# Performance work log

Measured on AMD Instinct MI355X. Metric: run time of the kernel, lower is better.

The kernel has to match this reference:

```python
import jax, jax.numpy as jnp
import numpy as np

D_MODEL = 512
N_HEADS = 8
EDGE_FEAT_DIM = 4
NUM_GRAPHS = 64
NODES_PER_GRAPH = 128
N_NODES = NUM_GRAPHS * NODES_PER_GRAPH          # 8192
EDGES_PER_GRAPH = 4096                           # avg degree 32
N_EDGES = NUM_GRAPHS * EDGES_PER_GRAPH           # 262144


def setup_inputs() -> dict:
    key = jax.random.key(0)
    ks = jax.random.split(key, 12)
    s = 0.02
    x = jax.random.normal(ks[0], (N_NODES, D_MODEL), jnp.float32)
    # edges constrained within their graph (block-diagonal structure)
    g_of_e = jnp.arange(N_EDGES, dtype=jnp.int32) // EDGES_PER_GRAPH
    src = g_of_e * NODES_PER_GRAPH + jax.random.randint(ks[1], (N_EDGES,), 0, NODES_PER_GRAPH, jnp.int32)
    dst = g_of_e * NODES_PER_GRAPH + jax.random.randint(ks[2], (N_EDGES,), 0, NODES_PER_GRAPH, jnp.int32)
    edge_index = jnp.stack([src, dst]).astype(jnp.int32)
    edge_attr = jax.random.normal(ks[3], (N_EDGES, EDGE_FEAT_DIM), jnp.float32)
    batch = jnp.repeat(jnp.arange(NUM_GRAPHS, dtype=jnp.int32), NODES_PER_GRAPH)
    # projection weights (in,out) convention: y = x @ W + b
    Wq = jax.random.normal(ks[4], (D_MODEL, D_MODEL), jnp.float32) * s
    Wk = jax.random.normal(ks[5], (D_MODEL, D_MODEL), jnp.float32) * s
    Wv = jax.random.normal(ks[6], (D_MODEL, D_MODEL), jnp.float32) * s
    Wo = jax.random.normal(ks[7], (D_MODEL, D_MODEL), jnp.float32) * s
    bq = jnp.zeros((D_MODEL,), jnp.float32)
    bk = jnp.zeros((D_MODEL,), jnp.float32)
    bv = jnp.zeros((D_MODEL,), jnp.float32)
    bo = jnp.zeros((D_MODEL,), jnp.float32)
    # edge bias MLP: edge_feat_dim -> d_model -> n_heads
    W1 = jax.random.normal(ks[8], (EDGE_FEAT_DIM, D_MODEL), jnp.float32) * s
    b1 = jnp.zeros((D_MODEL,), jnp.float32)
    W2 = jax.random.normal(ks[9], (D_MODEL, N_HEADS), jnp.float32) * s
    b2 = jnp.zeros((N_HEADS,), jnp.float32)
    return {"x": x, "edge_index": edge_index, "edge_attr": edge_attr, "batch": batch,
            "n_g": NODES_PER_GRAPH,
            "Wq": Wq, "bq": bq, "Wk": Wk, "bk": bk, "Wv": Wv, "bv": bv,
            "Wo": Wo, "bo": bo, "W1": W1, "b1": b1, "W2": W2, "b2": b2}


def reference(x, edge_index, edge_attr, batch, n_g, Wq, bq, Wk, bk, Wv, bv, Wo, bo, W1, b1, W2, b2):
    # batch is contiguous equal-size blocks of n_g nodes per graph, so the
    # per-graph Python loop of the original collapses to a batched (G, n_g)
    # block-diagonal attention. Dropout is identity (eval / p used only in train).
    N, d_model = x.shape
    H = W2.shape[1]
    d_k = d_model // H
    G = N // n_g
    scale = 1.0 / float(np.sqrt(d_k))

    Q = (x @ Wq + bq).reshape(G, n_g, H, d_k)
    K = (x @ Wk + bk).reshape(G, n_g, H, d_k)
    V = (x @ Wv + bv).reshape(G, n_g, H, d_k)

    # (G, i, j, h) dense per-graph scores
    scores = jnp.einsum('gihd,gjhd->gijh', Q, K) * scale

    # edge bias: MLP(edge_attr) -> (E, H), scattered at (graph, local_src, local_dst)
    bias = jax.nn.relu(edge_attr @ W1 + b1) @ W2 + b2
    ge = edge_index[0] // n_g
    ls = edge_index[0] % n_g
    ld = edge_index[1] % n_g
    scores = scores.at[ge, ls, ld].add(bias)

    attn = jax.nn.softmax(scores, axis=2)  # softmax over j (keys), matches dim=1 of (i,j,h)
    out = jnp.einsum('gijh,gjhd->gihd', attn, V).reshape(N, d_model)
    return out @ Wo + bo
```

## Files before the change

### kernel.cpp

```cpp
#include <hip/hip_runtime.h>
#include <hip/hip_bf16.h>

#define E_TOTAL 262144
#define NG      128
#define GRAPHS  64
#define NHEADS  8
#define DKH     64
#define DMODEL  512
#define NNODES  8192

typedef __bf16 bf16x8 __attribute__((ext_vector_type(8)));
typedef __bf16 bf16x4 __attribute__((ext_vector_type(4)));
typedef float  f32x4  __attribute__((ext_vector_type(4)));
typedef short  s16x4  __attribute__((ext_vector_type(4)));

typedef __attribute__((address_space(3))) char lds_char;
typedef const __attribute__((address_space(1))) char glb_char;

__device__ inline __hip_bfloat16 f2hbf(float f) { return __float2bfloat16(f); }
__device__ inline unsigned short f2u16(float f) {
    return __builtin_bit_cast(unsigned short, __float2bfloat16(f));
}
__device__ inline __bf16 f2bf(float f) {
    return __builtin_bit_cast(__bf16, f2u16(f));
}
__device__ inline bf16x8 cvt8(float4 lo, float4 hi) {
    bf16x8 o;
    o[0] = f2bf(lo.x); o[1] = f2bf(lo.y); o[2] = f2bf(lo.z); o[3] = f2bf(lo.w);
    o[4] = f2bf(hi.x); o[5] = f2bf(hi.y); o[6] = f2bf(hi.z); o[7] = f2bf(hi.w);
    return o;
}

__global__ __launch_bounds__(256) void prep_kernel(
    const float* __restrict__ Wq, const float* __restrict__ Wk,
    const float* __restrict__ Wv, const float* __restrict__ Wo,
    const float* __restrict__ W1, const float* __restrict__ b1,
    const float* __restrict__ W2, const float* __restrict__ b2,
    const float* __restrict__ x, __hip_bfloat16* __restrict__ xbf,
    __hip_bfloat16* __restrict__ wqkvt, __hip_bfloat16* __restrict__ wot,
    __hip_bfloat16* __restrict__ w1fragt, float* __restrict__ b1f,
    __hip_bfloat16* __restrict__ w2at, float* __restrict__ b2f)
{
    int blk = blockIdx.x, tid = threadIdx.x;
    if (blk < 256) {
        __shared__ __align__(16) __hip_bfloat16 tile[64][65];
        const float* src;
        __hip_bfloat16* dstT;
        int n0, k0, nb;
        if (blk < 192) {
            int nt = blk % 24, ktile = blk / 24;
            n0 = nt * 64; k0 = ktile * 64;
            if (n0 < 512)       { src = Wq; nb = n0; }
            else if (n0 < 1024) { src = Wk; nb = n0 - 512; }
            else                { src = Wv; nb = n0 - 1024; }
            dstT = wqkvt;
        } else {
            int t = blk - 192;
            n0 = (t % 8) * 64; k0 = (t / 8) * 64; nb = n0;
            src = Wo; dstT = wot;
        }
        #pragma unroll
        for (int i = 0; i < 16; ++i) {
            int idx = tid + i * 256;
            int kr = idx >> 6, nc = idx & 63;
            tile[kr][nc] = f2hbf(src[(size_t)(k0 + kr) * 512 + nb + nc]);
        }
        __syncthreads();
        #pragma unroll
        for (int i = 0; i < 16; ++i) {
            int idx = tid + i * 256;
            int nr = idx >> 6, kc = idx & 63;
            dstT[(size_t)(n0 + nr) * 512 + k0 + kc] = tile[kc][nr];
        }
    } else if (blk == 256) {
        __hip_bfloat16 z = f2hbf(0.f);
        for (int n = tid; n < 512; n += 256) {
            #pragma unroll
            for (int j = 0; j < 4; ++j) w1fragt[n * 4 + j] = f2hbf(W1[(size_t)j * 512 + n]);
        }
        for (int i = tid; i < 512; i += 256) b1f[i] = b1[i];
        for (int i = tid; i < 32 * 64 * 4; i += 256) {
            int t = i >> 8, lane = (i >> 2) & 63, j = i & 3;
            int q = lane >> 4, l = lane & 15;
            w2at[i] = (l < 8) ? f2hbf(W2[(size_t)(16 * t + 4 * q + j) * 8 + l]) : z;
        }
        if (tid < 8) b2f[tid] = b2[tid];
    } else {
        int base = (blk - 257) * 2048 + tid * 8;
        float4 lo = *(const float4*)(x + base);
        float4 hi = *(const float4*)(x + base + 4);
        *(bf16x8*)(xbf + base) = cvt8(lo, hi);
    }
}

template <bool QKPATH>
__device__ __forceinline__ void gemm0_body(
    const __hip_bfloat16* __restrict__ A, const __hip_bfloat16* __restrict__ BT,
    int row0, int col0,
    const float* __restrict__ bq, const float* __restrict__ bk,
    const float* __restrict__ bv,
    __hip_bfloat16* __restrict__ qbuf, __hip_bfloat16* __restrict__ kbuf,
    __hip_bfloat16* __restrict__ vt,
    __hip_bfloat16* __restrict__ As, __hip_bfloat16* __restrict__ Bs)
{
    const int K = 512;
    int tid = threadIdx.x;
    int lane = tid & 63, quad = lane >> 4, l16 = lane & 15;
    int wave = tid >> 6;
    int wi = wave >> 1, wj = wave & 1;

    f32x4 acc[2][4];
    #pragma unroll
    for (int a = 0; a < 2; a++)
        #pragma unroll
        for (int b = 0; b < 4; b++)
            #pragma unroll
            for (int r = 0; r < 4; r++) acc[a][b][r] = 0.f;

    const __hip_bfloat16* Ag = A + (size_t)(row0 + (tid >> 2)) * K + (tid & 3) * 8;
    const __hip_bfloat16* Bg = BT + (size_t)(col0 + (tid >> 2)) * K + (tid & 3) * 8;
    char* AsB = (char*)As;
    char* BsB = (char*)Bs;

#define G0STAGE(kt, buf) do { \
    __builtin_amdgcn_global_load_lds((glb_char*)(Ag + (kt) * 32), (lds_char*)(AsB + (buf) * 8192 + tid * 16), 16, 0, 0); \
    __builtin_amdgcn_global_load_lds((glb_char*)(Bg + (kt) * 32), (lds_char*)(BsB + (buf) * 8192 + tid * 16), 16, 0, 0); \
} while (0)

    G0STAGE(0, 0);
    G0STAGE(1, 1);

    #pragma unroll
    for (int kt = 0; kt < 16; ++kt) {
        if (kt < 15) asm volatile("s_waitcnt vmcnt(2)" ::: "memory");
        else         asm volatile("s_waitcnt vmcnt(0)" ::: "memory");
        __builtin_amdgcn_s_barrier();
        if (kt < 14) G0STAGE(kt + 2, (kt + 2) % 3);
        const __hip_bfloat16* Asc = As + (kt % 3) * 4096;
        const __hip_bfloat16* Bsc = Bs + (kt % 3) * 4096;
        bf16x8 af[2], bfr[4];
        #pragma unroll
        for (int t = 0; t < 2; t++)
            af[t] = *(const bf16x8*)&Asc[(wi * 32 + t * 16 + l16) * 32 + quad * 8];
        #pragma unroll
        for (int t = 0; t < 4; t++)
            bfr[t] = *(const bf16x8*)&Bsc[(wj * 64 + t * 16 + l16) * 32 + quad * 8];
        #pragma unroll
        for (int ti = 0; ti < 2; ti++)
            #pragma unroll
            for (int tj = 0; tj < 4; tj++) {
                if constexpr (QKPATH)
                    acc[ti][tj] = __builtin_amdgcn_mfma_f32_16x16x32_bf16(bfr[tj], af[ti], acc[ti][tj], 0, 0, 0);
                else
                    acc[ti][tj] = __builtin_amdgcn_mfma_f32_16x16x32_bf16(af[ti], bfr[tj], acc[ti][tj], 0, 0, 0);
            }
    }
#undef G0STAGE

    if constexpr (QKPATH) {
        int g = row0 >> 7;
        int ibase = wi * 32 + l16;
        int cb0 = col0 + wj * 64 + quad * 4;
        bool isQ = (col0 < 512);
        const float* bias = isQ ? bq : bk;
        int boff = isQ ? 0 : 512;
        __hip_bfloat16* dstbuf = isQ ? qbuf : kbuf;
        #pragma unroll
        for (int tj = 0; tj < 4; tj++) {
            int cb = cb0 + tj * 16;
            float4 bb = *(const float4*)(bias + cb - boff);
            int c = cb - boff;
            int hh = c >> 6, d = c & 63;
            __hip_bfloat16* dst = dstbuf + ((size_t)(g * 8 + hh) * 128) * 64 + d;
            #pragma unroll
            for (int ti = 0; ti < 2; ti++) {
                int i = ibase + ti * 16;
                bf16x4 v;
                v[0] = f2bf(acc[ti][tj][0] + bb.x);
                v[1] = f2bf(acc[ti][tj][1] + bb.y);
                v[2] = f2bf(acc[ti][tj][2] + bb.z);
                v[3] = f2bf(acc[ti][tj][3] + bb.w);
                *(bf16x4*)(dst + (size_t)i * 64) = v;
            }
        }
    } else {
        int g = row0 >> 7;
        int i0 = wi * 32 + quad * 4;
        #pragma unroll
        for (int tj = 0; tj < 4; tj++) {
            int c = col0 - 1024 + wj * 64 + tj * 16 + l16;
            int hh = c >> 6, d = c & 63;
            float bvv = bv[c];
            __hip_bfloat16* vdst = vt + ((size_t)(g * 8 + hh) * 64 + d) * 128 + i0;
            #pragma unroll
            for (int ti = 0; ti < 2; ti++) {
                bf16x4 v;
                v[0] = f2bf(acc[ti][tj][0] + bvv);
                v[1] = f2bf(acc[ti][tj][1] + bvv);
                v[2] = f2bf(acc[ti][tj][2] + bvv);
                v[3] = f2bf(acc[ti][tj][3] + bvv);
                *(bf16x4*)(vdst + ti * 16) = v;
            }
        }
    }
}

__device__ __forceinline__ void edge_body(
    int eblk,
    const float* __restrict__ ea,
    const __hip_bfloat16* __restrict__ w1fragt, const float* __restrict__ b1f,
    const __hip_bfloat16* __restrict__ w2at, const float* __restrict__ b2f,
    float* __restrict__ biasE)
{
    int tid = threadIdx.x, wave = tid >> 6, lane = tid & 63;
    int quad = lane >> 4, l16 = lane & 15;
    int eb = eblk * 512 + wave * 64;

    s16x4 eaf[4] = {};
    if (quad == 0) {
        #pragma unroll
        for (int gg = 0; gg < 4; ++gg) {
            float4 e4 = *(const float4*)(ea + (size_t)(eb + gg * 16 + l16) * 4);
            eaf[gg][0] = (short)f2u16(e4.x); eaf[gg][1] = (short)f2u16(e4.y);
            eaf[gg][2] = (short)f2u16(e4.z); eaf[gg][3] = (short)f2u16(e4.w);
        }
    }

    f32x4 c2[4];
    #pragma unroll
    for (int gg = 0; gg < 4; ++gg)
        #pragma unroll
        for (int r = 0; r < 4; ++r) c2[gg][r] = 0.f;

    #pragma unroll 4
    for (int t = 0; t < 32; ++t) {
        s16x4 a1 = *(const s16x4*)(w1fragt + ((size_t)t * 16 + l16) * 4);
        float4 b14 = *(const float4*)(b1f + t * 16 + quad * 4);
        s16x4 a2 = *(const s16x4*)(w2at + ((size_t)t * 64 + lane) * 4);
        #pragma unroll
        for (int gg = 0; gg < 4; ++gg) {
            f32x4 c1;
            c1[0] = b14.x; c1[1] = b14.y; c1[2] = b14.z; c1[3] = b14.w;
            c1 = __builtin_amdgcn_mfma_f32_16x16x16bf16_1k(a1, eaf[gg], c1, 0, 0, 0);
            s16x4 hfrag;
            hfrag[0] = (short)f2u16(fmaxf(c1[0], 0.f));
            hfrag[1] = (short)f2u16(fmaxf(c1[1], 0.f));
            hfrag[2] = (short)f2u16(fmaxf(c1[2], 0.f));
            hfrag[3] = (short)f2u16(fmaxf(c1[3], 0.f));
            c2[gg] = __builtin_amdgcn_mfma_f32_16x16x16bf16_1k(a2, hfrag, c2[gg], 0, 0, 0);
        }
    }
    if (quad < 2) {
        #pragma unroll
        for (int gg = 0; gg < 4; ++gg) {
            #pragma unroll
            for (int r = 0; r < 4; ++r) {
                int hh = quad * 4 + r;
                biasE[(size_t)hh * E_TOTAL + eb + gg * 16 + l16] = c2[gg][r] + b2f[hh];
            }
        }
    }
}

__global__ __launch_bounds__(512) void mega_kernel(
    const __hip_bfloat16* __restrict__ A, const __hip_bfloat16* __restrict__ BT,
    const float* __restrict__ bq, const float* __restrict__ bk,
    const float* __restrict__ bv,
    __hip_bfloat16* __restrict__ qbuf, __hip_bfloat16* __restrict__ kbuf,
    __hip_bfloat16* __restrict__ vt,
    const float* __restrict__ ea,
    const __hip_bfloat16* __restrict__ w1fragt, const float* __restrict__ b1f,
    const __hip_bfloat16* __restrict__ w2at, const float* __restrict__ b2f,
    float* __restrict__ biasE)
{
    __shared__ __align__(16) __hip_bfloat16 As[3 * 128 * 32];
    __shared__ __align__(16) __hip_bfloat16 Bs[3 * 128 * 32];
    int blk = blockIdx.x;
    int u = blk / 5, v = blk % 5;
    if (v < 3) {
        int tile = u * 3 + v;
        int row0 = (tile & 63) * 128, col0 = (tile >> 6) * 128;
        if (col0 < 1024)
            gemm0_body<true>(A, BT, row0, col0, bq, bk, bv, qbuf, kbuf, vt, As, Bs);
        else
            gemm0_body<false>(A, BT, row0, col0, bq, bk, bv, qbuf, kbuf, vt, As, Bs);
    } else {
        edge_body(u * 2 + (v - 3), ea, w1fragt, b1f, w2at, b2f, biasE);
    }
}

__global__ __launch_bounds__(256) void gemm1_kernel(
    const __hip_bfloat16* __restrict__ A, const __hip_bfloat16* __restrict__ BT,
    const float* __restrict__ bo, float* __restrict__ out)
{
    const int K = 512;
    __shared__ __align__(16) __hip_bfloat16 As[3 * 128 * 32];
    __shared__ __align__(16) __hip_bfloat16 Bs[3 * 64 * 32];
    int tid = threadIdx.x;
    int lane = tid & 63, quad = lane >> 4, l16 = lane & 15;
    int wave = tid >> 6, wi = wave >> 1, wj = wave & 1;
    int row0 = blockIdx.x * 128, col0 = blockIdx.y * 64;

    f32x4 acc[4][2];
    #pragma unroll
    for (int a = 0; a < 4; a++)
        #pragma unroll
        for (int b = 0; b < 2; b++)
            #pragma unroll
            for (int r = 0; r < 4; r++) acc[a][b][r] = 0.f;

    const __hip_bfloat16* Ag0 = A + (size_t)(row0 + (tid >> 2)) * K + (tid & 3) * 8;
    const __hip_bfloat16* Ag1 = Ag0 + (size_t)64 * K;
    const __hip_bfloat16* Bg  = BT + (size_t)(col0 + (tid >> 2)) * K + (tid & 3) * 8;
    char* AsB = (char*)As;
    char* BsB = (char*)Bs;

#define G1STAGE(kt, buf) do { \
    __builtin_amdgcn_global_load_lds((glb_char*)(Ag0 + (kt) * 32), (lds_char*)(AsB + (buf) * 8192 + tid * 16), 16, 0, 0); \
    __builtin_amdgcn_global_load_lds((glb_char*)(Ag1 + (kt) * 32), (lds_char*)(AsB + (buf) * 8192 + 4096 + tid * 16), 16, 0, 0); \
    __builtin_amdgcn_global_load_lds((glb_char*)(Bg + (kt) * 32),  (lds_char*)(BsB + (buf) * 4096 + tid * 16), 16, 0, 0); \
} while (0)

    G1STAGE(0, 0);
    G1STAGE(1, 1);

    #pragma unroll
    for (int kt = 0; kt < 16; ++kt) {
        if (kt < 15) asm volatile("s_waitcnt vmcnt(3)" ::: "memory");
        else         asm volatile("s_waitcnt vmcnt(0)" ::: "memory");
        __builtin_amdgcn_s_barrier();
        if (kt < 14) G1STAGE(kt + 2, (kt + 2) % 3);
        const __hip_bfloat16* Asc = As + (kt % 3) * 4096;
        const __hip_bfloat16* Bsc = Bs + (kt % 3) * 2048;
        bf16x8 af[4], bfr[2];
        #pragma unroll
        for (int t = 0; t < 4; t++)
            af[t] = *(const bf16x8*)&Asc[(wi * 64 + t * 16 + l16) * 32 + quad * 8];
        #pragma unroll
        for (int t = 0; t < 2; t++)
            bfr[t] = *(const bf16x8*)&Bsc[(wj * 32 + t * 16 + l16) * 32 + quad * 8];
        #pragma unroll
        for (int ti = 0; ti < 4; ti++)
            #pragma unroll
            for (int tj = 0; tj < 2; tj++)
                acc[ti][tj] = __builtin_amdgcn_mfma_f32_16x16x32_bf16(bfr[tj], af[ti], acc[ti][tj], 0, 0, 0);
    }
#undef G1STAGE

    int rbase = row0 + wi * 64 + l16;
    int cb0 = col0 + wj * 32 + quad * 4;
    #pragma unroll
    for (int tj = 0; tj < 2; tj++) {
        int cb = cb0 + tj * 16;
        float4 bb = *(const float4*)(bo + cb);
        #pragma unroll
        for (int ti = 0; ti < 4; ti++) {
            int row = rbase + ti * 16;
            f32x4 v;
            v[0] = acc[ti][tj][0] + bb.x;
            v[1] = acc[ti][tj][1] + bb.y;
            v[2] = acc[ti][tj][2] + bb.z;
            v[3] = acc[ti][tj][3] + bb.w;
            *(f32x4*)(out + (size_t)row * 512 + cb) = v;
        }
    }
}

#define SS 132
__global__ __launch_bounds__(512) void attn_kernel(
    const __hip_bfloat16* __restrict__ qbuf,
    const __hip_bfloat16* __restrict__ kbuf,
    const __hip_bfloat16* __restrict__ vt,
    const float* __restrict__ biasE,
    const int* __restrict__ eidx,
    __hip_bfloat16* __restrict__ O)
{
    __shared__ __align__(16) float S[128 * SS];
    int blk = blockIdx.x, g = blk & 63, h = blk >> 6;
    int tid = threadIdx.x, wave = tid >> 6, lane = tid & 63;
    int quad = lane >> 4, l16 = lane & 15;

    int   sa[8];
    float bvv[8];
    #pragma unroll
    for (int u = 0; u < 8; ++u) {
        int idx = g * 4096 + tid + u * 512;
        int ls = eidx[idx] & 127;
        int ld = eidx[E_TOTAL + idx] & 127;
        sa[u] = ls * SS + ld;
        bvv[u] = biasE[(size_t)h * E_TOTAL + idx];
    }

    const __hip_bfloat16* qbase = qbuf + (size_t)(g * 8 + h) * 128 * 64;
    const __hip_bfloat16* kbase = kbuf + (size_t)(g * 8 + h) * 128 * 64;
    const __hip_bfloat16* vbase = vt + (size_t)(g * 8 + h) * 64 * 128;

    f32x4 acc[8];
    #pragma unroll
    for (int j = 0; j < 8; j++)
        #pragma unroll
        for (int r = 0; r < 4; r++) acc[j][r] = 0.f;

    #pragma unroll
    for (int k0 = 0; k0 < 64; k0 += 32) {
        int m = wave * 16 + l16;
        bf16x8 af = *(const bf16x8*)(qbase + (size_t)m * 64 + k0 + quad * 8);
        #pragma unroll
        for (int tj = 0; tj < 8; tj++) {
            int n = tj * 16 + l16;
            bf16x8 bfr = *(const bf16x8*)(kbase + (size_t)n * 64 + k0 + quad * 8);
            acc[tj] = __builtin_amdgcn_mfma_f32_16x16x32_bf16(bfr, af, acc[tj], 0, 0, 0);
        }
    }
    {
        int i = wave * 16 + l16;
        #pragma unroll
        for (int tj = 0; tj < 8; tj++) {
            f32x4 sv;
            sv[0] = acc[tj][0] * 0.125f;
            sv[1] = acc[tj][1] * 0.125f;
            sv[2] = acc[tj][2] * 0.125f;
            sv[3] = acc[tj][3] * 0.125f;
            *(f32x4*)&S[i * SS + tj * 16 + quad * 4] = sv;
        }
    }

    bf16x8 vpre[8];
    #pragma unroll
    for (int kh = 0; kh < 2; kh++)
        #pragma unroll
        for (int tj = 0; tj < 4; tj++)
            vpre[kh * 4 + tj] = *(const bf16x8*)(vbase + (size_t)(tj * 16 + l16) * 128 + kh * 32 + quad * 8);

    __syncthreads();

    #pragma unroll
    for (int u = 0; u < 8; ++u)
        atomicAdd(&S[sa[u]], bvv[u]);
    __syncthreads();

    #pragma unroll 4
    for (int r = wave * 16; r < wave * 16 + 16; ++r) {
        float2 v = *(const float2*)&S[r * SS + 2 * lane];
        float m = fmaxf(v.x, v.y);
        #pragma unroll
        for (int off = 32; off > 0; off >>= 1) m = fmaxf(m, __shfl_xor(m, off));
        float e0 = __expf(v.x - m), e1 = __expf(v.y - m);
        float s = e0 + e1;
        #pragma unroll
        for (int off = 32; off > 0; off >>= 1) s += __shfl_xor(s, off);
        float inv = 1.0f / s;
        float2 o; o.x = e0 * inv; o.y = e1 * inv;
        *(float2*)&S[r * SS + 2 * lane] = o;
    }
    __syncthreads();

    f32x4 oacc[4];
    #pragma unroll
    for (int j = 0; j < 4; j++)
        #pragma unroll
        for (int r = 0; r < 4; r++) oacc[j][r] = 0.f;

    #pragma unroll
    for (int k0 = 0; k0 < 128; k0 += 32) {
        int m = wave * 16 + l16;
        const float* p = &S[m * SS + k0 + quad * 8];
        f32x4 xa = *(const f32x4*)p;
        f32x4 xb = *(const f32x4*)(p + 4);
        bf16x8 af;
        af[0] = f2bf(xa[0]); af[1] = f2bf(xa[1]); af[2] = f2bf(xa[2]); af[3] = f2bf(xa[3]);
        af[4] = f2bf(xb[0]); af[5] = f2bf(xb[1]); af[6] = f2bf(xb[2]); af[7] = f2bf(xb[3]);
        #pragma unroll
        for (int tj = 0; tj < 4; tj++) {
            bf16x8 bfr = (k0 < 64)
                ? vpre[(k0 >> 5) * 4 + tj]
                : *(const bf16x8*)(vbase + (size_t)(tj * 16 + l16) * 128 + k0 + quad * 8);
            oacc[tj] = __builtin_amdgcn_mfma_f32_16x16x32_bf16(bfr, af, oacc[tj], 0, 0, 0);
        }
    }
    {
        int i = wave * 16 + l16;
        __hip_bfloat16* obase = O + (size_t)(g * 128 + i) * 512 + h * 64 + quad * 4;
        #pragma unroll
        for (int tj = 0; tj < 4; tj++) {
            bf16x4 ov;
            ov[0] = f2bf(oacc[tj][0]);
            ov[1] = f2bf(oacc[tj][1]);
            ov[2] = f2bf(oacc[tj][2]);
            ov[3] = f2bf(oacc[tj][3]);
            *(bf16x4*)(obase + tj * 16) = ov;
        }
    }
}

#define WS_WQKVT 0x0
#define WS_WOT   0x180000
#define WS_W1FR  0x200000
#define WS_B1F   0x202000
#define WS_W2AT  0x202800
#define WS_B2F   0x206800
#define WS_Q     0x210000
#define WS_K     0xA10000
#define WS_VT    0x1210000
#define WS_BIASE 0x1A10000
#define WS_O     0x2210000
#define WS_XBF   WS_O

extern "C" void kernel_launch(void* const* d_in, const int* in_sizes, int n_in,
                              void* d_out, int out_size, void* d_ws, size_t ws_size,
                              hipStream_t stream) {
    const float* x    = (const float*)d_in[0];
    const int*   eidx = (const int*)d_in[1];
    const float* ea   = (const float*)d_in[2];
    const float* Wq = (const float*)d_in[5];
    const float* bq = (const float*)d_in[6];
    const float* Wk = (const float*)d_in[7];
    const float* bk = (const float*)d_in[8];
    const float* Wv = (const float*)d_in[9];
    const float* bv = (const float*)d_in[10];
    const float* Wo = (const float*)d_in[11];
    const float* bo = (const float*)d_in[12];
    const float* W1 = (const float*)d_in[13];
    const float* b1 = (const float*)d_in[14];
    const float* W2 = (const float*)d_in[15];
    const float* b2 = (const float*)d_in[16];

    char* ws = (char*)d_ws;
    __hip_bfloat16* wqkvt   = (__hip_bfloat16*)(ws + WS_WQKVT);
    __hip_bfloat16* wot     = (__hip_bfloat16*)(ws + WS_WOT);
    __hip_bfloat16* w1fragt = (__hip_bfloat16*)(ws + WS_W1FR);
    float* b1f   = (float*)(ws + WS_B1F);
    __hip_bfloat16* w2at    = (__hip_bfloat16*)(ws + WS_W2AT);
    float* b2f   = (float*)(ws + WS_B2F);
    __hip_bfloat16* qbuf = (__hip_bfloat16*)(ws + WS_Q);
    __hip_bfloat16* kbuf = (__hip_bfloat16*)(ws + WS_K);
    __hip_bfloat16* vt  = (__hip_bfloat16*)(ws + WS_VT);
    float* biasE = (float*)(ws + WS_BIASE);
    __hip_bfloat16* O   = (__hip_bfloat16*)(ws + WS_O);
    __hip_bfloat16* xbf = (__hip_bfloat16*)(ws + WS_XBF);

    prep_kernel<<<257 + 2048, 256, 0, stream>>>(Wq, Wk, Wv, Wo, W1, b1, W2, b2,
                                                x, xbf,
                                                wqkvt, wot, w1fragt, b1f, w2at, b2f);
    mega_kernel<<<1280, 512, 0, stream>>>(
        xbf, wqkvt, bq, bk, bv, qbuf, kbuf, vt,
        ea, w1fragt, b1f, w2at, b2f, biasE);
    attn_kernel<<<GRAPHS * NHEADS, 512, 0, stream>>>(qbuf, kbuf, vt, biasE, eidx, O);
    gemm1_kernel<<<dim3(NNODES / 128, 512 / 64), 256, 0, stream>>>(
        O, wot, bo, (float*)d_out);
}
```

Before: 200.0 us.

## Stage edge-MLP weight tables in LDS and remap mega-kernel block order

Edge-bias blocks now copy the packed W1 fragment, b1 and W2 tables (about 22 KB, laid out contiguously in the workspace) into shared memory, then run the MLP loop reading from LDS instead of global memory. The workspace offsets are compacted so the three tables sit back to back. Block IDs are also permuted with an interleave by 8, which changes how GEMM tiles and edge blocks are spread across XCDs and scheduled. The cost is an extra LDS fill plus a barrier per edge block, and the remap may change L2 locality for the GEMM tiles.

```diff
diff --git a/kernel.cpp b/kernel.cpp
--- a/kernel.cpp
+++ b/kernel.cpp
@@ -208,8 +208,8 @@
 __device__ __forceinline__ void edge_body(
     int eblk,
     const float* __restrict__ ea,
-    const __hip_bfloat16* __restrict__ w1fragt, const float* __restrict__ b1f,
-    const __hip_bfloat16* __restrict__ w2at, const float* __restrict__ b2f,
+    const __hip_bfloat16* w1s, const float* b1s, const __hip_bfloat16* w2s,
+    const float* __restrict__ b2f,
     float* __restrict__ biasE)
 {
     int tid = threadIdx.x, wave = tid >> 6, lane = tid & 63;
@@ -234,9 +234,9 @@
 
     #pragma unroll 4
     for (int t = 0; t < 32; ++t) {
-        s16x4 a1 = *(const s16x4*)(w1fragt + ((size_t)t * 16 + l16) * 4);
-        float4 b14 = *(const float4*)(b1f + t * 16 + quad * 4);
-        s16x4 a2 = *(const s16x4*)(w2at + ((size_t)t * 64 + lane) * 4);
+        s16x4 a1 = *(const s16x4*)(w1s + ((size_t)t * 16 + l16) * 4);
+        float4 b14 = *(const float4*)(b1s + t * 16 + quad * 4);
+        s16x4 a2 = *(const s16x4*)(w2s + ((size_t)t * 64 + lane) * 4);
         #pragma unroll
         for (int gg = 0; gg < 4; ++gg) {
             f32x4 c1;
@@ -269,13 +269,14 @@
     __hip_bfloat16* __restrict__ qbuf, __hip_bfloat16* __restrict__ kbuf,
     __hip_bfloat16* __restrict__ vt,
     const float* __restrict__ ea,
-    const __hip_bfloat16* __restrict__ w1fragt, const float* __restrict__ b1f,
-    const __hip_bfloat16* __restrict__ w2at, const float* __restrict__ b2f,
+    const char* __restrict__ tabg,
+    const float* __restrict__ b2f,
     float* __restrict__ biasE)
 {
     __shared__ __align__(16) __hip_bfloat16 As[3 * 128 * 32];
     __shared__ __align__(16) __hip_bfloat16 Bs[3 * 128 * 32];
-    int blk = blockIdx.x;
+    int blk0 = blockIdx.x;
+    int blk = (blk0 & 7) * 160 + (blk0 >> 3);
     int u = blk / 5, v = blk % 5;
     if (v < 3) {
         int tile = u * 3 + v;
@@ -285,7 +286,19 @@
         else
             gemm0_body<false>(A, BT, row0, col0, bq, bk, bv, qbuf, kbuf, vt, As, Bs);
     } else {
-        edge_body(u * 2 + (v - 3), ea, w1fragt, b1f, w2at, b2f, biasE);
+        int tid = threadIdx.x;
+        int4* dst = (int4*)As;
+        const int4* srcv = (const int4*)tabg;
+        #pragma unroll
+        for (int i = 0; i < 3; ++i) {
+            int idx = tid + i * 512;
+            if (idx < 1408) dst[idx] = srcv[idx];
+        }
+        __syncthreads();
+        const __hip_bfloat16* w1s = (const __hip_bfloat16*)As;
+        const float* b1s = (const float*)((const char*)As + 0x1000);
+        const __hip_bfloat16* w2s = (const __hip_bfloat16*)((const char*)As + 0x1800);
+        edge_body(u * 2 + (v - 3), ea, w1s, b1s, w2s, b2f, biasE);
     }
 }
 
@@ -495,10 +508,11 @@
 
 #define WS_WQKVT 0x0
 #define WS_WOT   0x180000
+#define WS_TAB   0x200000
 #define WS_W1FR  0x200000
-#define WS_B1F   0x202000
-#define WS_W2AT  0x202800
-#define WS_B2F   0x206800
+#define WS_B1F   0x201000
+#define WS_W2AT  0x201800
+#define WS_B2F   0x205800
 #define WS_Q     0x210000
 #define WS_K     0xA10000
 #define WS_VT    0x1210000
@@ -544,7 +558,7 @@
                                                 wqkvt, wot, w1fragt, b1f, w2at, b2f);
     mega_kernel<<<1280, 512, 0, stream>>>(
         xbf, wqkvt, bq, bk, bv, qbuf, kbuf, vt,
-        ea, w1fragt, b1f, w2at, b2f, biasE);
+        ea, ws + WS_TAB, b2f, biasE);
     attn_kernel<<<GRAPHS * NHEADS, 512, 0, stream>>>(qbuf, kbuf, vt, biasE, eidx, O);
     gemm1_kernel<<<dim3(NNODES / 128, 512 / 64), 256, 0, stream>>>(
         O, wot, bo, (float*)d_out);
```

Result: faster. 195.8 us (-2.1%).
